# Kernel optimization log

Measured on AMD Instinct MI355X. Metric: run time of the kernel, lower is better.

## Reference

```python
import jax, jax.numpy as jnp
import numpy as np
import math

B, S, IN_DIM, FEATURES = 4, 4096, 1024, 1024


def setup_inputs() -> dict:
    key = jax.random.key(0)
    kx, kk = jax.random.split(key)
    x = jax.random.normal(kx, (B, S, IN_DIM), dtype=jnp.float32)
    # bool kernel representing a +1/-1 binary weight matrix
    kernel = jax.random.randint(kk, (IN_DIM, FEATURES), 0, 2).astype(jnp.bool_)
    scale = jnp.float32(1.0 / math.sqrt(IN_DIM))  # nn.initializers.constant(1/sqrt(in_dim))
    return {"x": x, "kernel": kernel, "scale": scale}


def reference(x, kernel, scale):
    # conn_dense: bool kernel encodes +1 (True) / -1 (False) weights
    w = jnp.where(kernel, 1.0, -1.0).astype(x.dtype)  # [in_dim, features]
    # [b, s, in] @ [in, f] -> [b, s, f], then scalar scale
    return scale * jnp.einsum("bsi,if->bsf", x, w)
```

## Files before the change

### kernel.cpp

```cpp
#include <hip/hip_runtime.h>


#define M_TOT 16384
#define N_TOT 1024
#define K_TOT 1024

typedef __attribute__((ext_vector_type(8))) short bf16x8;
typedef __attribute__((ext_vector_type(4))) float f32x4;

__device__ __forceinline__ unsigned short f2bf(float f) {
    unsigned int u = __builtin_bit_cast(unsigned int, f);
    u += 0x7FFFu + ((u >> 16) & 1u);
    return (unsigned short)(u >> 16);
}

__device__ __forceinline__ unsigned int cvt_pk_bf16(float lo, float hi) {
    unsigned int r;
    asm("v_cvt_pk_bf16_f32 %0, %1, %2" : "=v"(r) : "v"(lo), "v"(hi));
    return r;
}

__global__ void detect_mode(const unsigned int* __restrict__ k32, int* __restrict__ flag) {
    __shared__ int s;
    if (threadIdx.x == 0) s = 0;
    __syncthreads();
    int bad = 0;
    for (int i = threadIdx.x; i < 1024; i += 256)
        if (k32[i] > 1u) bad = 1;
    if (bad) atomicOr(&s, 1);
    __syncthreads();
    if (threadIdx.x == 0) flag[0] = s;
}

__global__ __launch_bounds__(256) void convert_w(
    const void* __restrict__ w_raw, unsigned short* __restrict__ wt,
    const int* __restrict__ mode_p)
{
    __shared__ unsigned short tile[64 * 72];
    const int tid = threadIdx.x;
    const int k0 = (blockIdx.x & 15) * 64;
    const int n0 = (blockIdx.x >> 4) * 64;
    const int row = tid >> 2;
    const int seg = (tid & 3) * 16;

    if (mode_p[0] == 0) {
        const unsigned int* w = (const unsigned int*)w_raw;
        const uint4* src = reinterpret_cast<const uint4*>(
            w + (size_t)(k0 + row) * N_TOT + n0 + seg);
        #pragma unroll
        for (int q = 0; q < 4; ++q) {
            uint4 v = src[q];
            ushort4 h;
            h.x = v.x ? 0x3F80u : 0xBF80u;
            h.y = v.y ? 0x3F80u : 0xBF80u;
            h.z = v.z ? 0x3F80u : 0xBF80u;
            h.w = v.w ? 0x3F80u : 0xBF80u;
            *reinterpret_cast<ushort4*>(&tile[row * 72 + seg + q * 4]) = h;
        }
    } else {
        const unsigned char* w = (const unsigned char*)w_raw;
        uint4 v = *reinterpret_cast<const uint4*>(
            w + (size_t)(k0 + row) * N_TOT + n0 + seg);
        unsigned char b[16];
        *reinterpret_cast<uint4*>(b) = v;
        #pragma unroll
        for (int q = 0; q < 4; ++q) {
            ushort4 h;
            h.x = b[q * 4 + 0] ? 0x3F80u : 0xBF80u;
            h.y = b[q * 4 + 1] ? 0x3F80u : 0xBF80u;
            h.z = b[q * 4 + 2] ? 0x3F80u : 0xBF80u;
            h.w = b[q * 4 + 3] ? 0x3F80u : 0xBF80u;
            *reinterpret_cast<ushort4*>(&tile[row * 72 + seg + q * 4]) = h;
        }
    }
    __syncthreads();
    {
        int n = tid >> 2, kseg = (tid & 3) * 16;
        ushort4 o[4];
        #pragma unroll
        for (int j = 0; j < 16; ++j)
            ((unsigned short*)o)[j] = tile[(kseg + j) * 72 + n];
        ushort4* dst = reinterpret_cast<ushort4*>(wt + (size_t)(n0 + n) * K_TOT + k0 + kseg);
        dst[0] = o[0]; dst[1] = o[1]; dst[2] = o[2]; dst[3] = o[3];
    }
}

__global__ __launch_bounds__(256, 4) void fused_gemm(
    const float* __restrict__ X,
    const unsigned short* __restrict__ BT,
    const float* __restrict__ scale_p, float* __restrict__ out)
{
    __shared__ unsigned short As[128 * 64];
    __shared__ unsigned short Bs[128 * 64];

    const int tid  = threadIdx.x;
    const int lane = tid & 63;
    const int wave = tid >> 6;
    const int wm = (wave & 1) * 64;
    const int wn = (wave >> 1) * 64;

    const int j  = blockIdx.x & 7;
    const int s  = blockIdx.x >> 3;
    const int by = ((s >> 3) << 3) | j;
    const int bx = s & 7;
    const int m0 = by * 128, n0 = bx * 128;

    const int fr = lane & 15, fq = lane >> 4;
    const float scale = scale_p[0];

    const int srow_l = lane >> 3;
    const int gch    = lane & 7;
    const int lch    = gch ^ srow_l;
    const int skch   = gch ^ srow_l;

    f32x4 acc[4][4] = {};

    for (int k0 = 0; k0 < K_TOT; k0 += 64) {
        #pragma unroll
        for (int q = 0; q < 4; ++q) {
            const unsigned short* g = BT + (size_t)(n0 + wave * 32 + q * 8 + srow_l) * K_TOT
                                         + k0 + skch * 8;
            __builtin_amdgcn_global_load_lds(
                (const __attribute__((address_space(1))) void*)g,
                (__attribute__((address_space(3))) void*)&Bs[wave * 2048 + q * 512],
                16, 0, 0);
        }
        #pragma unroll
        for (int q = 0; q < 4; ++q) {
            const int r = wave * 32 + q * 8 + srow_l;
            const float4* g = reinterpret_cast<const float4*>(
                X + (size_t)(m0 + r) * K_TOT + k0 + gch * 8);
            float4 va = g[0];
            float4 vb = g[1];
            uint4 p;
            p.x = cvt_pk_bf16(va.x, va.y);
            p.y = cvt_pk_bf16(va.z, va.w);
            p.z = cvt_pk_bf16(vb.x, vb.y);
            p.w = cvt_pk_bf16(vb.z, vb.w);
            *reinterpret_cast<uint4*>(&As[r * 64 + lch * 8]) = p;
        }
        __syncthreads();

        #pragma unroll
        for (int ks = 0; ks < 2; ++ks) {
            bf16x8 af[4], bfr[4];
            #pragma unroll
            for (int mi = 0; mi < 4; ++mi) {
                int r  = wm + mi * 16 + fr;
                int ch = (ks * 4 + fq) ^ (r & 7);
                af[mi] = *reinterpret_cast<const bf16x8*>(&As[r * 64 + ch * 8]);
            }
            #pragma unroll
            for (int ni = 0; ni < 4; ++ni) {
                int r  = wn + ni * 16 + fr;
                int ch = (ks * 4 + fq) ^ (r & 7);
                bfr[ni] = *reinterpret_cast<const bf16x8*>(&Bs[r * 64 + ch * 8]);
            }
            #pragma unroll
            for (int mi = 0; mi < 4; ++mi)
                #pragma unroll
                for (int ni = 0; ni < 4; ++ni)
                    acc[mi][ni] = __builtin_amdgcn_mfma_f32_16x16x32_bf16(
                        af[mi], bfr[ni], acc[mi][ni], 0, 0, 0);
        }
        __syncthreads();
    }

    #pragma unroll
    for (int mi = 0; mi < 4; ++mi) {
        #pragma unroll
        for (int ni = 0; ni < 4; ++ni) {
            const int col  = n0 + wn + ni * 16 + fr;
            const int rowb = m0 + wm + mi * 16 + fq * 4;
            #pragma unroll
            for (int jj = 0; jj < 4; ++jj)
                out[(size_t)(rowb + jj) * N_TOT + col] = scale * acc[mi][ni][jj];
        }
    }
}

#define BKP 40
__global__ __launch_bounds__(256, 2) void binary_dense_gemm(
    const float* __restrict__ x, const int* __restrict__ kern,
    const float* __restrict__ scale_p, float* __restrict__ out)
{
    __shared__ unsigned short Asf[128 * BKP];
    __shared__ unsigned short Bsf[128 * BKP];
    const int tid = threadIdx.x, lane = tid & 63, wave = tid >> 6;
    const int wm = (wave & 1) * 64, wn = (wave >> 1) * 64;
    const int bx = blockIdx.x & 7, by = blockIdx.x >> 3;
    const int m0 = by * 128, n0 = bx * 128;
    const float scale = scale_p[0];
    const int fr = lane & 15, fq = lane >> 4;
    f32x4 acc[4][4] = {};
    for (int k0 = 0; k0 < K_TOT; k0 += 32) {
        #pragma unroll
        for (int i = 0; i < 4; ++i) {
            int slot = tid + i * 256, row = slot >> 3, kg = (slot & 7) << 2;
            const float4 v = *reinterpret_cast<const float4*>(x + (size_t)(m0 + row) * K_TOT + k0 + kg);
            ushort4 h;
            h.x = f2bf(v.x); h.y = f2bf(v.y); h.z = f2bf(v.z); h.w = f2bf(v.w);
            *reinterpret_cast<ushort4*>(&Asf[row * BKP + kg]) = h;
        }
        #pragma unroll
        for (int i = 0; i < 4; ++i) {
            int slot = tid + i * 256, nl = slot & 127, kg = (slot >> 7) << 2;
            ushort4 h;
            h.x = kern[(size_t)(k0 + kg + 0) * N_TOT + n0 + nl] ? 0x3F80u : 0xBF80u;
            h.y = kern[(size_t)(k0 + kg + 1) * N_TOT + n0 + nl] ? 0x3F80u : 0xBF80u;
            h.z = kern[(size_t)(k0 + kg + 2) * N_TOT + n0 + nl] ? 0x3F80u : 0xBF80u;
            h.w = kern[(size_t)(k0 + kg + 3) * N_TOT + n0 + nl] ? 0x3F80u : 0xBF80u;
            *reinterpret_cast<ushort4*>(&Bsf[nl * BKP + kg]) = h;
        }
        __syncthreads();
        bf16x8 af[4], bfr[4];
        #pragma unroll
        for (int mi = 0; mi < 4; ++mi)
            af[mi] = *reinterpret_cast<const bf16x8*>(&Asf[(wm + mi * 16 + fr) * BKP + fq * 8]);
        #pragma unroll
        for (int ni = 0; ni < 4; ++ni)
            bfr[ni] = *reinterpret_cast<const bf16x8*>(&Bsf[(wn + ni * 16 + fr) * BKP + fq * 8]);
        #pragma unroll
        for (int mi = 0; mi < 4; ++mi)
            #pragma unroll
            for (int ni = 0; ni < 4; ++ni)
                acc[mi][ni] = __builtin_amdgcn_mfma_f32_16x16x32_bf16(af[mi], bfr[ni], acc[mi][ni], 0, 0, 0);
        __syncthreads();
    }
    #pragma unroll
    for (int mi = 0; mi < 4; ++mi)
        #pragma unroll
        for (int ni = 0; ni < 4; ++ni) {
            const int col = n0 + wn + ni * 16 + fr;
            const int rowb = m0 + wm + mi * 16 + fq * 4;
            #pragma unroll
            for (int jj = 0; jj < 4; ++jj)
                out[(size_t)(rowb + jj) * N_TOT + col] = scale * acc[mi][ni][jj];
        }
}

extern "C" void kernel_launch(void* const* d_in, const int* in_sizes, int n_in,
                              void* d_out, int out_size, void* d_ws, size_t ws_size,
                              hipStream_t stream) {
    const float* x     = (const float*)d_in[0];
    const void*  kern  = d_in[1];
    const float* scale = (const float*)d_in[2];
    float*       out   = (float*)d_out;

    const size_t wt_bytes = (size_t)N_TOT * K_TOT * 2;
    const size_t flag_off = 256;
    if (ws_size >= flag_off + wt_bytes) {
        int*            flag = (int*)d_ws;
        unsigned short* wt   = (unsigned short*)((char*)d_ws + flag_off);
        hipLaunchKernelGGL(detect_mode, dim3(1), dim3(256), 0, stream,
                           (const unsigned int*)kern, flag);
        hipLaunchKernelGGL(convert_w, dim3(256), dim3(256), 0, stream, kern, wt, flag);
        hipLaunchKernelGGL(fused_gemm, dim3(1024), dim3(256), 0, stream,
                           x, wt, scale, out);
    } else {
        hipLaunchKernelGGL(binary_dense_gemm, dim3(1024), dim3(256), 0, stream,
                           x, (const int*)kern, scale, out);
    }
}
```

Before: 185.3 us.

## Double-buffer B tile and register-prefetch X in GEMM; fold mode detection into convert

The GEMM main loop now prefetches the next X tile into registers and the next B tile into a second LDS buffer while the current tile's fragments are consumed by MFMA, so global-load latency overlaps compute. The separate detect_mode kernel is removed and its check is done inside each convert_w block, saving one launch at the cost of redundant reads per block. The X conversion switches from the packed hardware bf16 instruction to a software rounding helper. The occupancy hint is dropped and register use rises from holding the prefetched floats and two fragment sets.

Result: faster. 166.6 us (-10.1%).

```diff
diff --git a/kernel.cpp b/kernel.cpp
--- a/kernel.cpp
+++ b/kernel.cpp
@@ -14,36 +14,29 @@
     return (unsigned short)(u >> 16);
 }
 
-__device__ __forceinline__ unsigned int cvt_pk_bf16(float lo, float hi) {
-    unsigned int r;
-    asm("v_cvt_pk_bf16_f32 %0, %1, %2" : "=v"(r) : "v"(lo), "v"(hi));
-    return r;
-}
-
-__global__ void detect_mode(const unsigned int* __restrict__ k32, int* __restrict__ flag) {
-    __shared__ int s;
-    if (threadIdx.x == 0) s = 0;
-    __syncthreads();
-    int bad = 0;
-    for (int i = threadIdx.x; i < 1024; i += 256)
-        if (k32[i] > 1u) bad = 1;
-    if (bad) atomicOr(&s, 1);
-    __syncthreads();
-    if (threadIdx.x == 0) flag[0] = s;
-}
-
 __global__ __launch_bounds__(256) void convert_w(
-    const void* __restrict__ w_raw, unsigned short* __restrict__ wt,
-    const int* __restrict__ mode_p)
+    const void* __restrict__ w_raw, unsigned short* __restrict__ wt)
 {
     __shared__ unsigned short tile[64 * 72];
+    __shared__ int smode;
     const int tid = threadIdx.x;
     const int k0 = (blockIdx.x & 15) * 64;
     const int n0 = (blockIdx.x >> 4) * 64;
     const int row = tid >> 2;
     const int seg = (tid & 3) * 16;
 
-    if (mode_p[0] == 0) {
+    if (tid == 0) smode = 0;
+    __syncthreads();
+    {
+        const unsigned int* k32 = (const unsigned int*)w_raw;
+        int bad = 0;
+        for (int i = tid; i < 1024; i += 256)
+            bad |= (k32[i] > 1u) ? 1 : 0;
+        if (bad) atomicOr(&smode, 1);
+    }
+    __syncthreads();
+
+    if (smode == 0) {
         const unsigned int* w = (const unsigned int*)w_raw;
         const uint4* src = reinterpret_cast<const uint4*>(
             w + (size_t)(k0 + row) * N_TOT + n0 + seg);
@@ -85,13 +78,13 @@
     }
 }
 
-__global__ __launch_bounds__(256, 4) void fused_gemm(
+__global__ __launch_bounds__(256) void fused_gemm(
     const float* __restrict__ X,
     const unsigned short* __restrict__ BT,
     const float* __restrict__ scale_p, float* __restrict__ out)
 {
     __shared__ unsigned short As[128 * 64];
-    __shared__ unsigned short Bs[128 * 64];
+    __shared__ unsigned short Bs[2][128 * 64];
 
     const int tid  = threadIdx.x;
     const int lane = tid & 63;
@@ -112,57 +105,86 @@
     const int gch    = lane & 7;
     const int lch    = gch ^ srow_l;
     const int skch   = gch ^ srow_l;
+    const int arow   = wave * 32 + srow_l;
 
     f32x4 acc[4][4] = {};
-
-    for (int k0 = 0; k0 < K_TOT; k0 += 64) {
+    float4 va[4], vb[4];
+
+    #pragma unroll
+    for (int q = 0; q < 4; ++q) {
+        const float4* g = reinterpret_cast<const float4*>(
+            X + (size_t)(m0 + arow + q * 8) * K_TOT + gch * 8);
+        va[q] = g[0];
+        vb[q] = g[1];
+    }
+    #pragma unroll
+    for (int q = 0; q < 4; ++q) {
+        const unsigned short* g = BT + (size_t)(n0 + arow + q * 8) * K_TOT + skch * 8;
+        __builtin_amdgcn_global_load_lds(
+            (const __attribute__((address_space(1))) void*)g,
+            (__attribute__((address_space(3))) void*)&Bs[0][wave * 2048 + q * 512],
+            16, 0, 0);
+    }
+
+    for (int t = 0; t < 16; ++t) {
+        const int cur = t & 1;
+
         #pragma unroll
         for (int q = 0; q < 4; ++q) {
-            const unsigned short* g = BT + (size_t)(n0 + wave * 32 + q * 8 + srow_l) * K_TOT
-                                         + k0 + skch * 8;
-            __builtin_amdgcn_global_load_lds(
-                (const __attribute__((address_space(1))) void*)g,
-                (__attribute__((address_space(3))) void*)&Bs[wave * 2048 + q * 512],
-                16, 0, 0);
-        }
-        #pragma unroll
-        for (int q = 0; q < 4; ++q) {
-            const int r = wave * 32 + q * 8 + srow_l;
-            const float4* g = reinterpret_cast<const float4*>(
-                X + (size_t)(m0 + r) * K_TOT + k0 + gch * 8);
-            float4 va = g[0];
-            float4 vb = g[1];
             uint4 p;
-            p.x = cvt_pk_bf16(va.x, va.y);
-            p.y = cvt_pk_bf16(va.z, va.w);
-            p.z = cvt_pk_bf16(vb.x, vb.y);
-            p.w = cvt_pk_bf16(vb.z, vb.w);
-            *reinterpret_cast<uint4*>(&As[r * 64 + lch * 8]) = p;
-        }
-        __syncthreads();
-
+            p.x = (unsigned)f2bf(va[q].x) | ((unsigned)f2bf(va[q].y) << 16);
+            p.y = (unsigned)f2bf(va[q].z) | ((unsigned)f2bf(va[q].w) << 16);
+            p.z = (unsigned)f2bf(vb[q].x) | ((unsigned)f2bf(vb[q].y) << 16);
+            p.w = (unsigned)f2bf(vb[q].z) | ((unsigned)f2bf(vb[q].w) << 16);
+            *reinterpret_cast<uint4*>(&As[(arow + q * 8) * 64 + lch * 8]) = p;
+        }
+        __syncthreads();
+
+        bf16x8 af[2][4], bfr[2][4];
         #pragma unroll
         for (int ks = 0; ks < 2; ++ks) {
-            bf16x8 af[4], bfr[4];
             #pragma unroll
             for (int mi = 0; mi < 4; ++mi) {
                 int r  = wm + mi * 16 + fr;
                 int ch = (ks * 4 + fq) ^ (r & 7);
-                af[mi] = *reinterpret_cast<const bf16x8*>(&As[r * 64 + ch * 8]);
+                af[ks][mi] = *reinterpret_cast<const bf16x8*>(&As[r * 64 + ch * 8]);
             }
             #pragma unroll
             for (int ni = 0; ni < 4; ++ni) {
                 int r  = wn + ni * 16 + fr;
                 int ch = (ks * 4 + fq) ^ (r & 7);
-                bfr[ni] = *reinterpret_cast<const bf16x8*>(&Bs[r * 64 + ch * 8]);
-            }
+                bfr[ks][ni] = *reinterpret_cast<const bf16x8*>(&Bs[cur][r * 64 + ch * 8]);
+            }
+        }
+
+        if (t < 15) {
+            const int kn = (t + 1) * 64;
+            #pragma unroll
+            for (int q = 0; q < 4; ++q) {
+                const float4* g = reinterpret_cast<const float4*>(
+                    X + (size_t)(m0 + arow + q * 8) * K_TOT + kn + gch * 8);
+                va[q] = g[0];
+                vb[q] = g[1];
+            }
+            #pragma unroll
+            for (int q = 0; q < 4; ++q) {
+                const unsigned short* g = BT + (size_t)(n0 + arow + q * 8) * K_TOT + kn + skch * 8;
+                __builtin_amdgcn_global_load_lds(
+                    (const __attribute__((address_space(1))) void*)g,
+                    (__attribute__((address_space(3))) void*)&Bs[cur ^ 1][wave * 2048 + q * 512],
+                    16, 0, 0);
+            }
+        }
+
+        #pragma unroll
+        for (int ks = 0; ks < 2; ++ks)
             #pragma unroll
             for (int mi = 0; mi < 4; ++mi)
                 #pragma unroll
                 for (int ni = 0; ni < 4; ++ni)
                     acc[mi][ni] = __builtin_amdgcn_mfma_f32_16x16x32_bf16(
-                        af[mi], bfr[ni], acc[mi][ni], 0, 0, 0);
-        }
+                        af[ks][mi], bfr[ks][ni], acc[mi][ni], 0, 0, 0);
+
         __syncthreads();
     }
 
@@ -248,13 +270,10 @@
     float*       out   = (float*)d_out;
 
     const size_t wt_bytes = (size_t)N_TOT * K_TOT * 2;
-    const size_t flag_off = 256;
-    if (ws_size >= flag_off + wt_bytes) {
-        int*            flag = (int*)d_ws;
-        unsigned short* wt   = (unsigned short*)((char*)d_ws + flag_off);
-        hipLaunchKernelGGL(detect_mode, dim3(1), dim3(256), 0, stream,
-                           (const unsigned int*)kern, flag);
-        hipLaunchKernelGGL(convert_w, dim3(256), dim3(256), 0, stream, kern, wt, flag);
+    const size_t wt_off   = 256;
+    if (ws_size >= wt_off + wt_bytes) {
+        unsigned short* wt = (unsigned short*)((char*)d_ws + wt_off);
+        hipLaunchKernelGGL(convert_w, dim3(256), dim3(256), 0, stream, kern, wt);
         hipLaunchKernelGGL(fused_gemm, dim3(1024), dim3(256), 0, stream,
                            x, wt, scale, out);
     } else {
```
